# Kernel tuning notes

Hardware: AMD Instinct MI355X
Metric: run time of the kernel (lower is better)

Reference implementation:

```python
import jax, jax.numpy as jnp
import numpy as np

EPS = 1e-5
K = 31  # large depthwise kernel
PAD = K // 2


def _bn(x, gamma, beta, mean, var):
    # x: [B, C, L]; params: [C]
    inv = gamma / jnp.sqrt(var + EPS)
    return x * inv[:, None] + (beta - mean * inv)[:, None]


def setup_inputs() -> dict:
    key = jax.random.key(0)
    ks = jax.random.split(key, 20)
    B, C, L = 32, 256, 4096
    H = 512  # hidden = C * expand_ratio(2)

    def bn_params(k, ch):
        k1, k2, k3, k4 = jax.random.split(k, 4)
        return (jax.random.normal(k1, (ch,)) * 0.1 + 1.0,   # gamma
                jax.random.normal(k2, (ch,)) * 0.1,          # beta
                jax.random.normal(k3, (ch,)) * 0.1,          # running mean
                jax.random.uniform(k4, (ch,)) * 0.5 + 0.5)   # running var

    g0, b0, m0, v0 = bn_params(ks[0], C)
    g1, b1, m1, v1 = bn_params(ks[1], H)
    g2, b2, m2, v2 = bn_params(ks[2], H)
    g3, b3, m3, v3 = bn_params(ks[3], C)

    return {
        "x": jax.random.normal(ks[4], (B, C, L), dtype=jnp.float32),
        "w_expand": jax.random.normal(ks[5], (H, C), dtype=jnp.float32) * (1.0 / np.sqrt(C)),
        "w_dw": jax.random.normal(ks[6], (H, 1, K), dtype=jnp.float32) * (1.0 / np.sqrt(K)),
        "w_project": jax.random.normal(ks[7], (C, H), dtype=jnp.float32) * (1.0 / np.sqrt(H)),
        "g0": g0, "b0": b0, "m0": m0, "v0": v0,
        "g1": g1, "b1": b1, "m1": m1, "v1": v1,
        "g2": g2, "b2": b2, "m2": m2, "v2": v2,
        "g3": g3, "b3": b3, "m3": m3, "v3": v3,
    }


def reference(x, w_expand, w_dw, w_project,
              g0, b0, m0, v0, g1, b1, m1, v1,
              g2, b2, m2, v2, g3, b3, m3, v3):
    shortcut = x
    # pre-norm BN
    h = _bn(x, g0, b0, m0, v0)
    # pw_expand: 1x1 conv (GEMM) + BN + ReLU -> [B, H, L]
    h = jnp.einsum("bcl,hc->bhl", h, w_expand)
    h = jax.nn.relu(_bn(h, g1, b1, m1, v1))
    # large-kernel depthwise conv + BN
    H = w_dw.shape[0]
    h = jax.lax.conv_general_dilated(
        h, w_dw, window_strides=(1,), padding=[(PAD, PAD)],
        dimension_numbers=("NCH", "OIH", "NCH"), feature_group_count=H)
    h = _bn(h, g2, b2, m2, v2)
    # activation then pw_project: 1x1 conv + BN -> [B, C, L]
    h = jax.nn.relu(h)
    h = jnp.einsum("bhl,ch->bcl", h, w_project)
    h = _bn(h, g3, b3, m3, v3)
    return shortcut + h  # drop_path=0 -> identity
```

## Files before the change

kernel.cpp:

```cpp
#include <hip/hip_runtime.h>
#include <hip/hip_bf16.h>

#define C_DIM 256
#define L_DIM 4096
#define H_DIM 512
#define KW    31
#define PADW  15

typedef unsigned short u16;
typedef unsigned int   u32;
typedef short bf16x8 __attribute__((ext_vector_type(8)));
typedef float f32x4  __attribute__((ext_vector_type(4)));

__device__ __forceinline__ u16 f2bf(float f) {
    u32 u = __float_as_uint(f);
    u32 r = (u + 0x7FFFu + ((u >> 16) & 1u)) >> 16;
    return (u16)r;
}
__device__ __forceinline__ float bf2f(u16 h) {
    return __uint_as_float(((u32)h) << 16);
}

typedef __attribute__((address_space(1))) const unsigned int gq_t;
typedef __attribute__((address_space(3))) unsigned int lq_t;
__device__ __forceinline__ void async16(void* lds, const void* g) {
    __builtin_amdgcn_global_load_lds((gq_t*)g, (lq_t*)lds, 16, 0, 0);
}

__global__ __launch_bounds__(256) void prep_kernel(
    const float* __restrict__ w_expand,
    const float* __restrict__ g0, const float* __restrict__ b0,
    const float* __restrict__ m0, const float* __restrict__ v0,
    const float* __restrict__ g1, const float* __restrict__ b1,
    const float* __restrict__ m1, const float* __restrict__ v1,
    const float* __restrict__ g2, const float* __restrict__ b2,
    const float* __restrict__ m2, const float* __restrict__ v2,
    const float* __restrict__ g3, const float* __restrict__ b3,
    const float* __restrict__ m3, const float* __restrict__ v3,
    u16* __restrict__ W0bf, float* __restrict__ A1, float* __restrict__ B1,
    float* __restrict__ A2, float* __restrict__ B2,
    float* __restrict__ A3, float* __restrict__ B3)
{
    __shared__ float red[256];
    const int h = blockIdx.x;
    const int c = threadIdx.x;

    float inv0 = g0[c] / sqrtf(v0[c] + 1e-5f);
    float add0 = b0[c] - m0[c] * inv0;
    float w = w_expand[h * C_DIM + c];
    W0bf[h * C_DIM + c] = f2bf(w * inv0);
    red[c] = add0 * w;
    __syncthreads();
    for (int s = 128; s > 0; s >>= 1) {
        if (c < s) red[c] += red[c + s];
        __syncthreads();
    }
    if (c == 0) {
        float bias0 = red[0];
        float inv1 = g1[h] / sqrtf(v1[h] + 1e-5f);
        A1[h] = inv1;
        B1[h] = bias0 * inv1 + (b1[h] - m1[h] * inv1);
        float inv2 = g2[h] / sqrtf(v2[h] + 1e-5f);
        A2[h] = inv2;
        B2[h] = b2[h] - m2[h] * inv2;
        if (h < C_DIM) {
            float inv3 = g3[h] / sqrtf(v3[h] + 1e-5f);
            A3[h] = inv3;
            B3[h] = b3[h] - m3[h] * inv3;
        }
    }
}

__global__ __launch_bounds__(256) void convw_kernel(
    const float* __restrict__ w, u16* __restrict__ o, int n)
{
    int i = blockIdx.x * 256 + threadIdx.x;
    if (i < n) o[i] = f2bf(w[i]);
}

__global__ __launch_bounds__(64) void prep2_kernel(
    const float* __restrict__ w_dw, u16* __restrict__ tab)
{
    const int h = blockIdx.x;
    const int lane = threadIdx.x;
    const int l15 = lane & 15, kg = lane >> 4;
    u16* dA = tab + ((size_t)h * 64 + lane) * 8;
    u16* dB = tab + (size_t)H_DIM * 64 * 8 + ((size_t)h * 64 + lane) * 8;
#pragma unroll
    for (int j = 0; j < 8; ++j) {
        int m1 = kg * 8 + j - l15 - 1;
        int m2 = m1 + 32;
        dA[j] = (m1 >= 0 && m1 < KW) ? f2bf(w_dw[h * KW + m1]) : (u16)0;
        dB[j] = (m2 >= 0 && m2 < KW) ? f2bf(w_dw[h * KW + m2]) : (u16)0;
    }
}

__global__ __launch_bounds__(256) void convx_kernel(
    const float* __restrict__ x, u16* __restrict__ xT)
{
    __shared__ u16 t_s[64][68];
    const int b = blockIdx.z, c0 = blockIdx.y * 64, l0 = blockIdx.x * 64;
    const int tid = threadIdx.x;
    const float* xb = x + (size_t)b * C_DIM * L_DIM;
    {
        const int cl = tid >> 2, lg = (tid & 3) * 16;
        const float* src = xb + (size_t)(c0 + cl) * L_DIM + l0 + lg;
#pragma unroll
        for (int j = 0; j < 16; j += 4) {
            float4 v = *(const float4*)(src + j);
            ushort4 o;
            o.x = f2bf(v.x); o.y = f2bf(v.y); o.z = f2bf(v.z); o.w = f2bf(v.w);
            *(ushort4*)&t_s[cl][lg + j] = o;
        }
    }
    __syncthreads();
    {
        const int ll = tid >> 2, cg = (tid & 3) * 16;
        u32 w0[4], w1[4];
#pragma unroll
        for (int j = 0; j < 4; ++j) {
            w0[j] = (u32)t_s[cg + 2*j][ll] | ((u32)t_s[cg + 2*j + 1][ll] << 16);
            w1[j] = (u32)t_s[cg + 8 + 2*j][ll] | ((u32)t_s[cg + 9 + 2*j][ll] << 16);
        }
        u16* dst = xT + ((size_t)b * L_DIM + l0 + ll) * C_DIM + c0 + cg;
        uint4 o0; o0.x = w0[0]; o0.y = w0[1]; o0.z = w0[2]; o0.w = w0[3];
        uint4 o1; o1.x = w1[0]; o1.y = w1[1]; o1.z = w1[2]; o1.w = w1[3];
        *(uint4*)(dst)     = o0;
        *(uint4*)(dst + 8) = o1;
    }
}

template<int KDIM, int EPI>
__global__ __launch_bounds__(256) void gemm_bt_kernel(
    const u16* __restrict__ A,
    const u16* __restrict__ BT,
    void* __restrict__ Out,
    const float* __restrict__ Sa, const float* __restrict__ Sb,
    const float* __restrict__ Xs)
{
    __shared__ short Asm[128 * 64];
    __shared__ short Bsm[128 * 64];
    const int b = blockIdx.z;
    const int bm = blockIdx.y * 128;
    const int bn = blockIdx.x * 128;
    const int tid = threadIdx.x;
    const int wave = tid >> 6, lane = tid & 63;
    const int wr = wave >> 1, wc = wave & 1;
    const int l15 = lane & 15, kg = lane >> 4;

    const u16* Bb = BT + (size_t)b * L_DIM * KDIM;

    const int srow = wave * 32 + (lane >> 3);
    const int scol = (lane & 7) * 8;
    const u16* gA = A  + (size_t)(bm + srow) * KDIM + scol;
    const u16* gB = Bb + (size_t)(bn + srow) * KDIM + scol;
    short* lA = Asm + wave * 32 * 64;
    short* lB = Bsm + wave * 32 * 64;

    f32x4 acc[4][4] = {};

    for (int kt = 0; kt < KDIM / 64; ++kt) {
        __syncthreads();
#pragma unroll
        for (int j = 0; j < 4; ++j) {
            async16(lA + j * 8 * 64, gA + (size_t)j * 8 * KDIM);
            async16(lB + j * 8 * 64, gB + (size_t)j * 8 * KDIM);
        }
        gA += 64; gB += 64;
        __syncthreads();
#pragma unroll
        for (int ks = 0; ks < 2; ++ks) {
            bf16x8 af[4], bf[4];
#pragma unroll
            for (int m = 0; m < 4; ++m)
                af[m] = *(const bf16x8*)&Asm[(wr * 64 + m * 16 + l15) * 64 + ks * 32 + kg * 8];
#pragma unroll
            for (int n = 0; n < 4; ++n)
                bf[n] = *(const bf16x8*)&Bsm[(wc * 64 + n * 16 + l15) * 64 + ks * 32 + kg * 8];
#pragma unroll
            for (int m = 0; m < 4; ++m)
#pragma unroll
                for (int n = 0; n < 4; ++n)
                    acc[m][n] = __builtin_amdgcn_mfma_f32_16x16x32_bf16(
                        af[m], bf[n], acc[m][n], 0, 0, 0);
        }
    }

    const int orow0 = bm + wr * 64;
    const int ocol = bn + wc * 64 + l15;
    if constexpr (EPI == 0) {
        u16* O = (u16*)Out + (size_t)b * H_DIM * L_DIM;
#pragma unroll
        for (int m = 0; m < 4; ++m)
#pragma unroll
        for (int r = 0; r < 4; ++r) {
            const int row = orow0 + m * 16 + kg * 4 + r;
            const float s = Sa[row], t = Sb[row];
#pragma unroll
            for (int n = 0; n < 4; ++n) {
                float v = acc[m][n][r] * s + t;
                v = v > 0.f ? v : 0.f;
                O[(size_t)row * L_DIM + ocol + n * 16] = f2bf(v);
            }
        }
    } else {
        float* O = (float*)Out + (size_t)b * C_DIM * L_DIM;
        const float* X = Xs + (size_t)b * C_DIM * L_DIM;
#pragma unroll
        for (int m = 0; m < 4; ++m)
#pragma unroll
        for (int r = 0; r < 4; ++r) {
            const int row = orow0 + m * 16 + kg * 4 + r;
            const float s = Sa[row], t = Sb[row];
#pragma unroll
            for (int n = 0; n < 4; ++n) {
                float v = acc[m][n][r] * s + t + X[(size_t)row * L_DIM + ocol + n * 16];
                O[(size_t)row * L_DIM + ocol + n * 16] = v;
            }
        }
    }
}

__global__ __launch_bounds__(256) void dw_kernel(
    const u16* __restrict__ h1, const u16* __restrict__ tab,
    u16* __restrict__ h2T,
    const float* __restrict__ A2, const float* __restrict__ B2)
{
    __shared__ u16 in_s[32][320];
    __shared__ u16 out_s[256][34];
    const int b = blockIdx.z, h0 = blockIdx.y * 32, l0 = blockIdx.x * 256;
    const int tid = threadIdx.x;
    const int wave = tid >> 6, lane = tid & 63;
    const int l15 = lane & 15, kg = lane >> 4;
    const u16* hb = h1 + (size_t)b * H_DIM * L_DIM;

#pragma unroll
    for (int it = 0; it < 5; ++it) {
        const int idx = tid + it * 256;
        const int r = idx / 40, g = idx % 40;
        const int bl = l0 - 16 + g * 8;
        const u16* src = hb + (size_t)(h0 + r) * L_DIM + bl;
        uint4 val;
        if (bl >= 0 && bl + 8 <= L_DIM) {
            val = *(const uint4*)src;
        } else {
            u16 t[8];
#pragma unroll
            for (int e = 0; e < 8; ++e)
                t[e] = (bl + e >= 0 && bl + e < L_DIM) ? src[e] : (u16)0;
            val.x = (u32)t[0] | ((u32)t[1] << 16);
            val.y = (u32)t[2] | ((u32)t[3] << 16);
            val.z = (u32)t[4] | ((u32)t[5] << 16);
            val.w = (u32)t[6] | ((u32)t[7] << 16);
        }
        *(uint4*)&in_s[r][g * 8] = val;
    }
    __syncthreads();

    const u16* tabB = tab + (size_t)H_DIM * 64 * 8;
    const int xoff = 16 * l15 + 8 * kg;
#pragma unroll
    for (int hp = 0; hp < 4; ++hp) {
        const int hlA = wave * 8 + hp * 2;
        const int hA = h0 + hlA, hB = hA + 1;
        bf16x8 a1A = *(const bf16x8*)(tab  + ((size_t)hA * 64 + lane) * 8);
        bf16x8 a2A = *(const bf16x8*)(tabB + ((size_t)hA * 64 + lane) * 8);
        bf16x8 a1B = *(const bf16x8*)(tab  + ((size_t)hB * 64 + lane) * 8);
        bf16x8 a2B = *(const bf16x8*)(tabB + ((size_t)hB * 64 + lane) * 8);
        bf16x8 x1A = *(const bf16x8*)&in_s[hlA][xoff];
        bf16x8 x2A = *(const bf16x8*)&in_s[hlA][xoff + 32];
        bf16x8 x1B = *(const bf16x8*)&in_s[hlA + 1][xoff];
        bf16x8 x2B = *(const bf16x8*)&in_s[hlA + 1][xoff + 32];
        f32x4 accA = {}, accB = {};
        accA = __builtin_amdgcn_mfma_f32_16x16x32_bf16(a1A, x1A, accA, 0, 0, 0);
        accA = __builtin_amdgcn_mfma_f32_16x16x32_bf16(a2A, x2A, accA, 0, 0, 0);
        accB = __builtin_amdgcn_mfma_f32_16x16x32_bf16(a1B, x1B, accB, 0, 0, 0);
        accB = __builtin_amdgcn_mfma_f32_16x16x32_bf16(a2B, x2B, accB, 0, 0, 0);
        const float sA = A2[hA], tA = B2[hA];
        const float sB = A2[hB], tB = B2[hB];
        const int c = wave * 4 + hp;
        const int lbase = 16 * l15 + 4 * kg;
#pragma unroll
        for (int r = 0; r < 4; ++r) {
            float vA = accA[r] * sA + tA; vA = vA > 0.f ? vA : 0.f;
            float vB = accB[r] * sB + tB; vB = vB > 0.f ? vB : 0.f;
            u32 pk;
            asm("v_cvt_pk_bf16_f32 %0, %1, %2" : "=v"(pk) : "v"(vA), "v"(vB));
            const int X = lbase + r;
            const int cp = c ^ ((X >> 4) & 3);
            *(u32*)&out_s[X][cp * 2] = pk;
        }
    }
    __syncthreads();

    u32 vals[16];
#pragma unroll
    for (int c = 0; c < 16; ++c) {
        const int cp = c ^ ((tid >> 4) & 3);
        vals[c] = *(const u32*)&out_s[tid][cp * 2];
    }
    u16* dst = h2T + ((size_t)b * L_DIM + l0 + tid) * H_DIM + h0;
#pragma unroll
    for (int q = 0; q < 4; ++q) {
        uint4 o;
        o.x = vals[q * 4 + 0]; o.y = vals[q * 4 + 1];
        o.z = vals[q * 4 + 2]; o.w = vals[q * 4 + 3];
        ((uint4*)dst)[q] = o;
    }
}

extern "C" void kernel_launch(void* const* d_in, const int* in_sizes, int n_in,
                              void* d_out, int out_size, void* d_ws, size_t ws_size,
                              hipStream_t stream) {
    const float* x        = (const float*)d_in[0];
    const float* w_expand = (const float*)d_in[1];
    const float* w_dw     = (const float*)d_in[2];
    const float* w_proj   = (const float*)d_in[3];
    const float* g0 = (const float*)d_in[4],  *b0 = (const float*)d_in[5];
    const float* m0 = (const float*)d_in[6],  *v0 = (const float*)d_in[7];
    const float* g1 = (const float*)d_in[8],  *b1 = (const float*)d_in[9];
    const float* m1 = (const float*)d_in[10], *v1 = (const float*)d_in[11];
    const float* g2 = (const float*)d_in[12], *b2 = (const float*)d_in[13];
    const float* m2 = (const float*)d_in[14], *v2 = (const float*)d_in[15];
    const float* g3 = (const float*)d_in[16], *b3 = (const float*)d_in[17];
    const float* m3 = (const float*)d_in[18], *v3 = (const float*)d_in[19];
    float* out = (float*)d_out;

    const int B = in_sizes[0] / (C_DIM * L_DIM);

    char* base = (char*)d_ws;
    size_t off = 0;
    u16* W0bf = (u16*)(base + off); off += (size_t)H_DIM * C_DIM * 2;
    u16* Wpbf = (u16*)(base + off); off += (size_t)C_DIM * H_DIM * 2;
    u16* tab  = (u16*)(base + off); off += (size_t)2 * H_DIM * 64 * 8 * 2;
    float* A1p = (float*)(base + off); off += H_DIM * 4;
    float* B1p = (float*)(base + off); off += H_DIM * 4;
    float* A2p = (float*)(base + off); off += H_DIM * 4;
    float* B2p = (float*)(base + off); off += H_DIM * 4;
    float* A3p = (float*)(base + off); off += C_DIM * 4;
    float* B3p = (float*)(base + off); off += C_DIM * 4;
    off = (off + 255) & ~(size_t)255;

    const size_t per_b = ((size_t)L_DIM * C_DIM + 2 * (size_t)H_DIM * L_DIM) * 2;
    int nb = 1;
    const int cands[6] = {32, 16, 8, 4, 2, 1};
    for (int i = 0; i < 6; ++i) {
        if (B % cands[i]) continue;
        if (off + per_b * cands[i] <= ws_size) { nb = cands[i]; break; }
    }
    u16* xT  = (u16*)(base + off);
    u16* h1  = xT + (size_t)nb * L_DIM * C_DIM;
    u16* h2T = h1 + (size_t)nb * H_DIM * L_DIM;

    prep_kernel<<<H_DIM, 256, 0, stream>>>(
        w_expand, g0, b0, m0, v0, g1, b1, m1, v1, g2, b2, m2, v2,
        g3, b3, m3, v3, W0bf, A1p, B1p, A2p, B2p, A3p, B3p);
    convw_kernel<<<(C_DIM * H_DIM + 255) / 256, 256, 0, stream>>>(
        w_proj, Wpbf, C_DIM * H_DIM);
    prep2_kernel<<<H_DIM, 64, 0, stream>>>(w_dw, tab);

    for (int cs = 0; cs < B; cs += nb) {
        const float* xb = x + (size_t)cs * C_DIM * L_DIM;
        float* ob = out + (size_t)cs * C_DIM * L_DIM;
        convx_kernel<<<dim3(L_DIM / 64, C_DIM / 64, nb), 256, 0, stream>>>(xb, xT);
        gemm_bt_kernel<C_DIM, 0><<<dim3(L_DIM / 128, H_DIM / 128, nb), 256, 0, stream>>>(
            W0bf, xT, h1, A1p, B1p, nullptr);
        dw_kernel<<<dim3(L_DIM / 256, H_DIM / 32, nb), 256, 0, stream>>>(
            h1, tab, h2T, A2p, B2p);
        gemm_bt_kernel<H_DIM, 1><<<dim3(L_DIM / 128, C_DIM / 128, nb), 256, 0, stream>>>(
            Wpbf, h2T, ob, A3p, B3p, xb);
    }
}
```

Measured before the change: 301.9 us.

## Swizzle GEMM LDS tiles and stage epilogue through shared memory for coalesced stores

Applies an XOR swizzle to the LDS layout of the A/B tiles in the bf16 GEMM to reduce bank conflicts on MFMA fragment reads. Both epilogues now stage results in shared memory and write out with wide 16-byte row-contiguous stores, and the residual add reads x as float4. The batch chunk size is also capped at 8 so intermediates stay smaller and more cache-resident. The cost is extra barriers and LDS round-trips in the epilogue.

```diff
diff --git a/kernel.cpp b/kernel.cpp
--- a/kernel.cpp
+++ b/kernel.cpp
@@ -138,8 +138,9 @@
     const float* __restrict__ Sa, const float* __restrict__ Sb,
     const float* __restrict__ Xs)
 {
-    __shared__ short Asm[128 * 64];
-    __shared__ short Bsm[128 * 64];
+    __shared__ short SH[2 * 128 * 64];
+    short* Asm = SH;
+    short* Bsm = SH + 128 * 64;
     const int b = blockIdx.z;
     const int bm = blockIdx.y * 128;
     const int bn = blockIdx.x * 128;
@@ -151,11 +152,13 @@
     const u16* Bb = BT + (size_t)b * L_DIM * KDIM;
 
     const int srow = wave * 32 + (lane >> 3);
-    const int scol = (lane & 7) * 8;
-    const u16* gA = A  + (size_t)(bm + srow) * KDIM + scol;
-    const u16* gB = Bb + (size_t)(bn + srow) * KDIM + scol;
+    const int scolb = ((lane & 7) * 16) ^ ((srow & 7) << 4);
+    const u16* gA = A  + (size_t)(bm + srow) * KDIM + (scolb >> 1);
+    const u16* gB = Bb + (size_t)(bn + srow) * KDIM + (scolb >> 1);
     short* lA = Asm + wave * 32 * 64;
     short* lB = Bsm + wave * 32 * 64;
+
+    const int rswz = (l15 & 7) << 4;
 
     f32x4 acc[4][4] = {};
 
@@ -173,10 +176,12 @@
             bf16x8 af[4], bf[4];
 #pragma unroll
             for (int m = 0; m < 4; ++m)
-                af[m] = *(const bf16x8*)&Asm[(wr * 64 + m * 16 + l15) * 64 + ks * 32 + kg * 8];
+                af[m] = *(const bf16x8*)((const char*)&Asm[(wr * 64 + m * 16 + l15) * 64]
+                                         + (((ks * 64 + kg * 16)) ^ rswz));
 #pragma unroll
             for (int n = 0; n < 4; ++n)
-                bf[n] = *(const bf16x8*)&Bsm[(wc * 64 + n * 16 + l15) * 64 + ks * 32 + kg * 8];
+                bf[n] = *(const bf16x8*)((const char*)&Bsm[(wc * 64 + n * 16 + l15) * 64]
+                                         + (((ks * 64 + kg * 16)) ^ rswz));
 #pragma unroll
             for (int m = 0; m < 4; ++m)
 #pragma unroll
@@ -186,36 +191,71 @@
         }
     }
 
-    const int orow0 = bm + wr * 64;
-    const int ocol = bn + wc * 64 + l15;
     if constexpr (EPI == 0) {
-        u16* O = (u16*)Out + (size_t)b * H_DIM * L_DIM;
+        __syncthreads();
+        char* osm = (char*)SH;
 #pragma unroll
         for (int m = 0; m < 4; ++m)
 #pragma unroll
         for (int r = 0; r < 4; ++r) {
-            const int row = orow0 + m * 16 + kg * 4 + r;
-            const float s = Sa[row], t = Sb[row];
+            const int row = wr * 64 + m * 16 + kg * 4 + r;
+            const int grow = bm + row;
+            const float s = Sa[grow], t = Sb[grow];
+            const int sw = (row & 7) << 4;
 #pragma unroll
             for (int n = 0; n < 4; ++n) {
+                const int col = wc * 64 + n * 16 + l15;
                 float v = acc[m][n][r] * s + t;
                 v = v > 0.f ? v : 0.f;
-                O[(size_t)row * L_DIM + ocol + n * 16] = f2bf(v);
+                *(u16*)(osm + row * 256 + ((col * 2) ^ sw)) = f2bf(v);
             }
+        }
+        __syncthreads();
+        const int row = tid >> 1, cb0 = (tid & 1) * 128;
+        const int sw = (row & 7) << 4;
+        u16* dst = (u16*)Out + (size_t)b * H_DIM * L_DIM
+                 + (size_t)(bm + row) * L_DIM + bn + (tid & 1) * 64;
+#pragma unroll
+        for (int q = 0; q < 8; ++q) {
+            uint4 v = *(const uint4*)(osm + row * 256 + ((cb0 + q * 16) ^ sw));
+            *(uint4*)(dst + q * 8) = v;
         }
     } else {
         float* O = (float*)Out + (size_t)b * C_DIM * L_DIM;
         const float* X = Xs + (size_t)b * C_DIM * L_DIM;
-#pragma unroll
-        for (int m = 0; m < 4; ++m)
-#pragma unroll
-        for (int r = 0; r < 4; ++r) {
-            const int row = orow0 + m * 16 + kg * 4 + r;
-            const float s = Sa[row], t = Sb[row];
-#pragma unroll
-            for (int n = 0; n < 4; ++n) {
-                float v = acc[m][n][r] * s + t + X[(size_t)row * L_DIM + ocol + n * 16];
-                O[(size_t)row * L_DIM + ocol + n * 16] = v;
+        char* osm = (char*)SH;
+#pragma unroll
+        for (int pass = 0; pass < 2; ++pass) {
+            __syncthreads();
+            if (wr == pass) {
+#pragma unroll
+                for (int m = 0; m < 4; ++m)
+#pragma unroll
+                for (int r = 0; r < 4; ++r) {
+                    const int rl = m * 16 + kg * 4 + r;
+                    const int grow = bm + pass * 64 + rl;
+                    const float s = Sa[grow], t = Sb[grow];
+                    const int sw = ((rl >> 2) & 3) << 6;
+#pragma unroll
+                    for (int n = 0; n < 4; ++n) {
+                        const int col = wc * 64 + n * 16 + l15;
+                        *(float*)(osm + rl * 512 + ((col * 4) ^ sw)) =
+                            acc[m][n][r] * s + t;
+                    }
+                }
+            }
+            __syncthreads();
+            const int rl = tid >> 2, c0 = (tid & 3) * 32;
+            const int grow = bm + pass * 64 + rl;
+            const int sw = ((rl >> 2) & 3) << 6;
+            float* dst = O + (size_t)grow * L_DIM + bn + c0;
+            const float* xs = X + (size_t)grow * L_DIM + bn + c0;
+#pragma unroll
+            for (int q = 0; q < 8; ++q) {
+                float4 v = *(const float4*)(osm + rl * 512 + (((c0 + q * 4) * 4) ^ sw));
+                float4 xv = *(const float4*)(xs + q * 4);
+                v.x += xv.x; v.y += xv.y; v.z += xv.z; v.w += xv.w;
+                *(float4*)(dst + q * 4) = v;
             }
         }
     }
@@ -343,8 +383,8 @@
 
     const size_t per_b = ((size_t)L_DIM * C_DIM + 2 * (size_t)H_DIM * L_DIM) * 2;
     int nb = 1;
-    const int cands[6] = {32, 16, 8, 4, 2, 1};
-    for (int i = 0; i < 6; ++i) {
+    const int cands[4] = {8, 4, 2, 1};
+    for (int i = 0; i < 4; ++i) {
         if (B % cands[i]) continue;
         if (off + per_b * cands[i] <= ws_size) { nb = cands[i]; break; }
     }
```

Measured after the change: 363.8 us. +20.5%, slower.

## Fuse fp32-to-bf16 transpose of x into the expand GEMM loader

Applied to the files above, without the earlier changes.

Drops the separate convx kernel that converted x to bf16 and transposed it into an [L,C] workspace. The expand GEMM now reads fp32 x directly, converts pairs of channels to packed bf16 and stores them transposed into shared memory. This removes one kernel launch plus the write and re-read of the xT buffer. The cost is synchronous global loads in the GEMM main loop instead of async copies for B. x is also re-read by each of the four H-tile blocks, and the strided LDS stores may bank-conflict.

```diff
diff --git a/kernel.cpp b/kernel.cpp
--- a/kernel.cpp
+++ b/kernel.cpp
@@ -95,46 +95,98 @@
     }
 }
 
-__global__ __launch_bounds__(256) void convx_kernel(
-    const float* __restrict__ x, u16* __restrict__ xT)
-{
-    __shared__ u16 t_s[64][68];
-    const int b = blockIdx.z, c0 = blockIdx.y * 64, l0 = blockIdx.x * 64;
+__global__ __launch_bounds__(256) void expand_fx_kernel(
+    const u16* __restrict__ W0bf,
+    const float* __restrict__ x,
+    u16* __restrict__ h1,
+    const float* __restrict__ A1, const float* __restrict__ B1)
+{
+    __shared__ short Asm[128 * 64];
+    __shared__ u32  Bsm[128][36];
+    const int b = blockIdx.z;
+    const int bn = blockIdx.x * 128;
+    const int bm = blockIdx.y * 128;
     const int tid = threadIdx.x;
+    const int wave = tid >> 6, lane = tid & 63;
+    const int wr = wave >> 1, wc = wave & 1;
+    const int l15 = lane & 15, kg = lane >> 4;
+
     const float* xb = x + (size_t)b * C_DIM * L_DIM;
-    {
-        const int cl = tid >> 2, lg = (tid & 3) * 16;
-        const float* src = xb + (size_t)(c0 + cl) * L_DIM + l0 + lg;
-#pragma unroll
-        for (int j = 0; j < 16; j += 4) {
-            float4 v = *(const float4*)(src + j);
-            ushort4 o;
-            o.x = f2bf(v.x); o.y = f2bf(v.y); o.z = f2bf(v.z); o.w = f2bf(v.w);
-            *(ushort4*)&t_s[cl][lg + j] = o;
-        }
-    }
-    __syncthreads();
-    {
-        const int ll = tid >> 2, cg = (tid & 3) * 16;
-        u32 w0[4], w1[4];
-#pragma unroll
-        for (int j = 0; j < 4; ++j) {
-            w0[j] = (u32)t_s[cg + 2*j][ll] | ((u32)t_s[cg + 2*j + 1][ll] << 16);
-            w1[j] = (u32)t_s[cg + 8 + 2*j][ll] | ((u32)t_s[cg + 9 + 2*j][ll] << 16);
-        }
-        u16* dst = xT + ((size_t)b * L_DIM + l0 + ll) * C_DIM + c0 + cg;
-        uint4 o0; o0.x = w0[0]; o0.y = w0[1]; o0.z = w0[2]; o0.w = w0[3];
-        uint4 o1; o1.x = w1[0]; o1.y = w1[1]; o1.z = w1[2]; o1.w = w1[3];
-        *(uint4*)(dst)     = o0;
-        *(uint4*)(dst + 8) = o1;
-    }
-}
-
-template<int KDIM, int EPI>
+
+    const int srow = wave * 32 + (lane >> 3);
+    const int scol = (lane & 7) * 8;
+    const u16* gA = W0bf + (size_t)(bm + srow) * C_DIM + scol;
+    short* lA = Asm + wave * 32 * 64;
+
+    const int cp = tid >> 5;
+    const int lg = tid & 31;
+
+    f32x4 acc[4][4] = {};
+
+    for (int kt = 0; kt < C_DIM / 64; ++kt) {
+        const int ck = kt * 64;
+        __syncthreads();
+#pragma unroll
+        for (int j = 0; j < 4; ++j)
+            async16(lA + j * 8 * 64, gA + (size_t)j * 8 * C_DIM);
+        gA += 64;
+#pragma unroll
+        for (int i = 0; i < 4; ++i) {
+            const int cpi = i * 8 + cp;
+            const float* s0 = xb + (size_t)(ck + 2 * cpi) * L_DIM + bn + lg * 4;
+            float4 va = *(const float4*)s0;
+            float4 vb = *(const float4*)(s0 + L_DIM);
+            u32 p0 = (u32)f2bf(va.x) | ((u32)f2bf(vb.x) << 16);
+            u32 p1 = (u32)f2bf(va.y) | ((u32)f2bf(vb.y) << 16);
+            u32 p2 = (u32)f2bf(va.z) | ((u32)f2bf(vb.z) << 16);
+            u32 p3 = (u32)f2bf(va.w) | ((u32)f2bf(vb.w) << 16);
+            Bsm[lg * 4 + 0][cpi] = p0;
+            Bsm[lg * 4 + 1][cpi] = p1;
+            Bsm[lg * 4 + 2][cpi] = p2;
+            Bsm[lg * 4 + 3][cpi] = p3;
+        }
+        __syncthreads();
+#pragma unroll
+        for (int ks = 0; ks < 2; ++ks) {
+            bf16x8 af[4], bf[4];
+#pragma unroll
+            for (int m = 0; m < 4; ++m)
+                af[m] = *(const bf16x8*)&Asm[(wr * 64 + m * 16 + l15) * 64 + ks * 32 + kg * 8];
+#pragma unroll
+            for (int n = 0; n < 4; ++n)
+                bf[n] = *(const bf16x8*)&Bsm[wc * 64 + n * 16 + l15][ks * 16 + kg * 4];
+#pragma unroll
+            for (int m = 0; m < 4; ++m)
+#pragma unroll
+                for (int n = 0; n < 4; ++n)
+                    acc[m][n] = __builtin_amdgcn_mfma_f32_16x16x32_bf16(
+                        af[m], bf[n], acc[m][n], 0, 0, 0);
+        }
+    }
+
+    const int orow0 = bm + wr * 64;
+    const int ocol = bn + wc * 64 + l15;
+    u16* O = h1 + (size_t)b * H_DIM * L_DIM;
+#pragma unroll
+    for (int m = 0; m < 4; ++m)
+#pragma unroll
+    for (int r = 0; r < 4; ++r) {
+        const int row = orow0 + m * 16 + kg * 4 + r;
+        const float s = A1[row], t = B1[row];
+#pragma unroll
+        for (int n = 0; n < 4; ++n) {
+            float v = acc[m][n][r] * s + t;
+            v = v > 0.f ? v : 0.f;
+            O[(size_t)row * L_DIM + ocol + n * 16] = f2bf(v);
+        }
+    }
+}
+
+template<int KDIM>
 __global__ __launch_bounds__(256) void gemm_bt_kernel(
     const u16* __restrict__ A,
     const u16* __restrict__ BT,
-    void* __restrict__ Out,
+    float* __restrict__ Out,
     const float* __restrict__ Sa, const float* __restrict__ Sb,
     const float* __restrict__ Xs)
 {
@@ -188,35 +240,18 @@
 
     const int orow0 = bm + wr * 64;
     const int ocol = bn + wc * 64 + l15;
-    if constexpr (EPI == 0) {
-        u16* O = (u16*)Out + (size_t)b * H_DIM * L_DIM;
-#pragma unroll
-        for (int m = 0; m < 4; ++m)
-#pragma unroll
-        for (int r = 0; r < 4; ++r) {
-            const int row = orow0 + m * 16 + kg * 4 + r;
-            const float s = Sa[row], t = Sb[row];
-#pragma unroll
-            for (int n = 0; n < 4; ++n) {
-                float v = acc[m][n][r] * s + t;
-                v = v > 0.f ? v : 0.f;
-                O[(size_t)row * L_DIM + ocol + n * 16] = f2bf(v);
-            }
-        }
-    } else {
-        float* O = (float*)Out + (size_t)b * C_DIM * L_DIM;
-        const float* X = Xs + (size_t)b * C_DIM * L_DIM;
-#pragma unroll
-        for (int m = 0; m < 4; ++m)
-#pragma unroll
-        for (int r = 0; r < 4; ++r) {
-            const int row = orow0 + m * 16 + kg * 4 + r;
-            const float s = Sa[row], t = Sb[row];
-#pragma unroll
-            for (int n = 0; n < 4; ++n) {
-                float v = acc[m][n][r] * s + t + X[(size_t)row * L_DIM + ocol + n * 16];
-                O[(size_t)row * L_DIM + ocol + n * 16] = v;
-            }
+    float* O = Out + (size_t)b * C_DIM * L_DIM;
+    const float* X = Xs + (size_t)b * C_DIM * L_DIM;
+#pragma unroll
+    for (int m = 0; m < 4; ++m)
+#pragma unroll
+    for (int r = 0; r < 4; ++r) {
+        const int row = orow0 + m * 16 + kg * 4 + r;
+        const float s = Sa[row], t = Sb[row];
+#pragma unroll
+        for (int n = 0; n < 4; ++n) {
+            float v = acc[m][n][r] * s + t + X[(size_t)row * L_DIM + ocol + n * 16];
+            O[(size_t)row * L_DIM + ocol + n * 16] = v;
         }
     }
 }
@@ -341,15 +376,14 @@
     float* B3p = (float*)(base + off); off += C_DIM * 4;
     off = (off + 255) & ~(size_t)255;
 
-    const size_t per_b = ((size_t)L_DIM * C_DIM + 2 * (size_t)H_DIM * L_DIM) * 2;
+    const size_t per_b = (size_t)2 * H_DIM * L_DIM * 2;
     int nb = 1;
     const int cands[6] = {32, 16, 8, 4, 2, 1};
     for (int i = 0; i < 6; ++i) {
         if (B % cands[i]) continue;
         if (off + per_b * cands[i] <= ws_size) { nb = cands[i]; break; }
     }
-    u16* xT  = (u16*)(base + off);
-    u16* h1  = xT + (size_t)nb * L_DIM * C_DIM;
+    u16* h1  = (u16*)(base + off);
     u16* h2T = h1 + (size_t)nb * H_DIM * L_DIM;
 
     prep_kernel<<<H_DIM, 256, 0, stream>>>(
@@ -362,12 +396,11 @@
     for (int cs = 0; cs < B; cs += nb) {
         const float* xb = x + (size_t)cs * C_DIM * L_DIM;
         float* ob = out + (size_t)cs * C_DIM * L_DIM;
-        convx_kernel<<<dim3(L_DIM / 64, C_DIM / 64, nb), 256, 0, stream>>>(xb, xT);
-        gemm_bt_kernel<C_DIM, 0><<<dim3(L_DIM / 128, H_DIM / 128, nb), 256, 0, stream>>>(
-            W0bf, xT, h1, A1p, B1p, nullptr);
+        expand_fx_kernel<<<dim3(L_DIM / 128, H_DIM / 128, nb), 256, 0, stream>>>(
+            W0bf, xb, h1, A1p, B1p);
         dw_kernel<<<dim3(L_DIM / 256, H_DIM / 32, nb), 256, 0, stream>>>(
             h1, tab, h2T, A2p, B2p);
-        gemm_bt_kernel<H_DIM, 1><<<dim3(L_DIM / 128, C_DIM / 128, nb), 256, 0, stream>>>(
+        gemm_bt_kernel<H_DIM><<<dim3(L_DIM / 128, C_DIM / 128, nb), 256, 0, stream>>>(
             Wpbf, h2T, ob, A3p, B3p, xb);
     }
 }
```

Result: slower. 337.9 us (+11.9%).
